# Optimization experiments

Measured on AMD Instinct MI355X. Metric: run time of the kernel, lower is better.

The kernel has to match this reference:

```python
import jax, jax.numpy as jnp
import numpy as np

B, N, EDGES = 16, 50000, 1600000
CLAMP_MIN, CLAMP_MAX = -10.0, 10.0
EPS = 1e-6


def setup_inputs() -> dict:
    key = jax.random.key(0)
    ks = jax.random.split(key, 8)
    return {
        "chem_influence": jax.random.normal(ks[0], (B, N), dtype=jnp.float32),
        "E": jax.random.normal(ks[1], (B, N), dtype=jnp.float32),
        "o_pre": jax.random.uniform(ks[2], (B, N), dtype=jnp.float32),
        "w": jax.random.normal(ks[3], (EDGES,), dtype=jnp.float32),
        "threshold": jax.random.uniform(ks[4], (N,), dtype=jnp.float32),
        "decay": jax.random.uniform(ks[5], (N,), dtype=jnp.float32),
        "src": jax.random.randint(ks[6], (EDGES,), 0, N, dtype=jnp.int32),
        "dst": jax.random.randint(ks[7], (EDGES,), 0, N, dtype=jnp.int32),
    }


def reference(chem_influence, E, o_pre, w, threshold, decay, src, dst):
    # Gap-junction currents: gather, sign-compare, weighted scatter-add.
    Oj = o_pre[:, src]                      # (B, EDGES) presynaptic outputs
    En = E[:, dst]                          # (B, EDGES) postsynaptic internal states
    sgn = jnp.where(Oj >= En, 1.0, -1.0)
    contrib = Oj * w * sgn                  # (B, EDGES)
    gj_sum = jnp.zeros_like(chem_influence).at[:, dst].add(contrib)  # (B, N)

    # Neuron dynamics (eqs 10, 11).
    S = jnp.clip(E + chem_influence + gj_sum, CLAMP_MIN, CLAMP_MAX)
    gt = S > threshold                      # broadcast (N,) over (B, N)
    mask = (~gt) & (jnp.abs(S - E) <= EPS)
    new_o = jax.nn.relu(S - threshold)
    new_e = jnp.where(gt, new_o, jnp.where(mask, E - decay, S))
    return (new_o, new_e)
```

## Files before the change

kernel.cpp:

```cpp
#include <hip/hip_runtime.h>

#define BATCH 16
#define NNODES 50000
#define NEDGES 1600000
#define BN (BATCH * NNODES)
#define NBLK 391
#define EPB 4096
#define BSZ 128
#define NBINS 391
#define CAPE 4992
#define RPT 10
#define CLAMP_LO -10.0f
#define CLAMP_HI 10.0f
#define EPS_V 1e-6f

__global__ __launch_bounds__(256) void prep_hist_kernel(
    const float* __restrict__ o_pre, const float* __restrict__ E,
    const int* __restrict__ dst,
    float* __restrict__ o_t, float* __restrict__ E_t,
    int* __restrict__ hist) {
    __shared__ int lh[NBINS];
    const int tid = threadIdx.x, bid = blockIdx.x;
    for (int i = tid; i < NBINS; i += 256) lh[i] = 0;

    if (tid < 128) {
        int t = bid * 128 + tid;
        if (t < NNODES) {
            float v[BATCH], u[BATCH];
#pragma unroll
            for (int b = 0; b < BATCH; ++b) {
                v[b] = o_pre[b * NNODES + t];
                u[b] = E[b * NNODES + t];
            }
            float4* op = (float4*)(o_t + (size_t)t * BATCH);
            float4* ep = (float4*)(E_t + (size_t)t * BATCH);
#pragma unroll
            for (int k = 0; k < 4; ++k) {
                op[k] = make_float4(v[4 * k], v[4 * k + 1], v[4 * k + 2], v[4 * k + 3]);
                ep[k] = make_float4(u[4 * k], u[4 * k + 1], u[4 * k + 2], u[4 * k + 3]);
            }
        }
    }
    __syncthreads();

    const int4* dst4 = (const int4*)dst;
    const int e4base = bid * (EPB / 4);
#pragma unroll
    for (int j = 0; j < 4; ++j) {
        int i4 = e4base + j * 256 + tid;
        if (i4 * 4 < NEDGES) {
            int4 d4 = dst4[i4];
            atomicAdd(&lh[d4.x >> 7], 1);
            atomicAdd(&lh[d4.y >> 7], 1);
            atomicAdd(&lh[d4.z >> 7], 1);
            atomicAdd(&lh[d4.w >> 7], 1);
        }
    }
    __syncthreads();
    for (int i = tid; i < NBINS; i += 256) hist[i * NBLK + bid] = lh[i];
}

__global__ __launch_bounds__(256) void scanA_kernel(int* __restrict__ hist,
                                                    int* __restrict__ totals) {
    __shared__ int sm[256];
    const int k = blockIdx.x, t = threadIdx.x;
    const int base = t * 2;
    int v0 = (base < NBLK) ? hist[k * NBLK + base] : 0;
    int v1 = (base + 1 < NBLK) ? hist[k * NBLK + base + 1] : 0;
    sm[t] = v0 + v1;
    __syncthreads();
    for (int off = 1; off < 256; off <<= 1) {
        int a = (t >= off) ? sm[t - off] : 0;
        __syncthreads();
        sm[t] += a;
        __syncthreads();
    }
    int run = (t > 0) ? sm[t - 1] : 0;
    if (base < NBLK) { hist[k * NBLK + base] = run; run += v0; }
    if (base + 1 < NBLK) hist[k * NBLK + base + 1] = run;
    if (t == 255) totals[k] = sm[255];
}

__global__ __launch_bounds__(256) void scatterA_kernel(
    const int* __restrict__ src, const int* __restrict__ dst,
    const float* __restrict__ w, const int* __restrict__ hist,
    uint2* __restrict__ binned) {
    __shared__ int cur[NBINS];
    const int tid = threadIdx.x, bid = blockIdx.x;
    for (int i = tid; i < NBINS; i += 256)
        cur[i] = i * CAPE + hist[i * NBLK + bid];
    __syncthreads();
    const int4*   dst4 = (const int4*)dst;
    const int4*   src4 = (const int4*)src;
    const float4* w4   = (const float4*)w;
    const int e4base = bid * (EPB / 4);
#pragma unroll
    for (int j = 0; j < 4; ++j) {
        int i4 = e4base + j * 256 + tid;
        if (i4 * 4 < NEDGES) {
            int4 d4 = dst4[i4];
            int4 s4 = src4[i4];
            float4 ww = w4[i4];
            int dd[4] = {d4.x, d4.y, d4.z, d4.w};
            int ss[4] = {s4.x, s4.y, s4.z, s4.w};
            float wv[4] = {ww.x, ww.y, ww.z, ww.w};
#pragma unroll
            for (int m = 0; m < 4; ++m) {
                int d = dd[m];
                int bin = d >> 7;
                int pos = atomicAdd(&cur[bin], 1);
                if (pos < (bin + 1) * CAPE)
                    binned[pos] = make_uint2(
                        (unsigned)ss[m] | ((unsigned)(d & 127) << 16),
                        __float_as_uint(wv[m]));
            }
        }
    }
}

__global__ __launch_bounds__(512) void bin_gather5(
    const float* __restrict__ o_t, const float* __restrict__ E_t,
    const float* __restrict__ chem, const float* __restrict__ threshold,
    const float* __restrict__ decay, const int* __restrict__ totals,
    const uint2* __restrict__ binned,
    float* __restrict__ out_o, float* __restrict__ out_e) {
    __shared__ int   cnt_l[BSZ];
    __shared__ int   offs[BSZ + 1];
    __shared__ int   sc[BSZ];
    __shared__ uint2 eb[CAPE];
    const int k = blockIdx.x, tid = threadIdx.x;
    const int node0 = k * BSZ;
    const int nn = (NNODES - node0 < BSZ) ? (NNODES - node0) : BSZ;
    const int s0 = k * CAPE;
    int cnt = totals[k];
    if (cnt > CAPE) cnt = CAPE;

    uint2 r[RPT];
    if (tid < BSZ) cnt_l[tid] = 0;
    __syncthreads();
#pragma unroll
    for (int j = 0; j < RPT; ++j) {
        int idx = tid + j * 512;
        if (idx < cnt) {
            uint2 p = binned[s0 + idx];
            r[j] = p;
            atomicAdd(&cnt_l[(p.x >> 16) & 127], 1);
        }
    }
    __syncthreads();

    if (tid < BSZ) sc[tid] = cnt_l[tid];
    __syncthreads();
    for (int o = 1; o < BSZ; o <<= 1) {
        int v = (tid >= o && tid < BSZ) ? sc[tid - o] : 0;
        __syncthreads();
        if (tid < BSZ) sc[tid] += v;
        __syncthreads();
    }
    if (tid < BSZ) {
        int ex = sc[tid] - cnt_l[tid];
        offs[tid] = ex;
        cnt_l[tid] = ex;
    }
    if (tid == 0) offs[BSZ] = cnt;
    __syncthreads();

#pragma unroll
    for (int j = 0; j < RPT; ++j) {
        int idx = tid + j * 512;
        if (idx < cnt) {
            uint2 p = r[j];
            int pos = atomicAdd(&cnt_l[(p.x >> 16) & 127], 1);
            if (pos < CAPE) eb[pos] = p;
        }
    }
    __syncthreads();

    for (int t = tid; t < nn * 4; t += 512) {
        int n = t >> 2;
        int q = (t & 3) * 4;
        int gn = node0 + n;
        int e0 = offs[n], e1 = offs[n + 1];
        float4 en = *(const float4*)(E_t + (size_t)gn * BATCH + q);
        float4 acc = make_float4(0.f, 0.f, 0.f, 0.f);
        for (int i = e0; i < e1; ++i) {
            uint2 p = eb[i];
            float wv = __uint_as_float(p.y);
            int s = (int)(p.x & 0xFFFFu);
            float4 oj = *(const float4*)(o_t + (size_t)s * BATCH + q);
            acc.x += (oj.x >= en.x) ? oj.x * wv : -oj.x * wv;
            acc.y += (oj.y >= en.y) ? oj.y * wv : -oj.y * wv;
            acc.z += (oj.z >= en.z) ? oj.z * wv : -oj.z * wv;
            acc.w += (oj.w >= en.w) ? oj.w * wv : -oj.w * wv;
        }
        float th = threshold[gn];
        float dc = decay[gn];
        float ev[4] = {en.x, en.y, en.z, en.w};
        float av[4] = {acc.x, acc.y, acc.z, acc.w};
#pragma unroll
        for (int j = 0; j < 4; ++j) {
            int b = q + j;
            float e = ev[j];
            float S = e + chem[b * NNODES + gn] + av[j];
            S = fminf(fmaxf(S, CLAMP_LO), CLAMP_HI);
            float no = fmaxf(S - th, 0.0f);
            float ne;
            if (S > th) ne = no;
            else if (fabsf(S - e) <= EPS_V) ne = e - dc;
            else ne = S;
            out_o[b * NNODES + gn] = no;
            out_e[b * NNODES + gn] = ne;
        }
    }
}

__global__ void edge_scatter_dev(const float* __restrict__ o_pre, const float* __restrict__ E,
                                 const float* __restrict__ w, const int* __restrict__ src,
                                 const int* __restrict__ dst, float* __restrict__ gj) {
    int e = blockIdx.x * blockDim.x + threadIdx.x;
    if (e >= NEDGES) return;
    int s = src[e];
    int d = dst[e];
    float wv = w[e];
#pragma unroll
    for (int b = 0; b < BATCH; ++b) {
        float oj = o_pre[b * NNODES + s];
        float en = E[b * NNODES + d];
        atomicAdd(&gj[b * NNODES + d], (oj >= en) ? oj * wv : -oj * wv);
    }
}

__global__ void finalize_dev(const float* __restrict__ chem, const float* __restrict__ E,
                             const float* __restrict__ threshold, const float* __restrict__ decay,
                             float* __restrict__ out_o, float* __restrict__ out_e_gj) {
    int i = blockIdx.x * blockDim.x + threadIdx.x;
    if (i >= BN) return;
    int n = i % NNODES;
    float e = E[i];
    float S = e + chem[i] + out_e_gj[i];
    S = fminf(fmaxf(S, CLAMP_LO), CLAMP_HI);
    float th = threshold[n];
    float no = fmaxf(S - th, 0.0f);
    float ne;
    if (S > th) ne = no;
    else if (fabsf(S - e) <= EPS_V) ne = e - decay[n];
    else ne = S;
    out_o[i] = no;
    out_e_gj[i] = ne;
}

extern "C" void kernel_launch(void* const* d_in, const int* in_sizes, int n_in,
                              void* d_out, int out_size, void* d_ws, size_t ws_size,
                              hipStream_t stream) {
    const float* chem      = (const float*)d_in[0];
    const float* E         = (const float*)d_in[1];
    const float* o_pre     = (const float*)d_in[2];
    const float* w         = (const float*)d_in[3];
    const float* threshold = (const float*)d_in[4];
    const float* decay     = (const float*)d_in[5];
    const int*   src       = (const int*)d_in[6];
    const int*   dst       = (const int*)d_in[7];

    float* out_o = (float*)d_out;
    float* out_e = (float*)d_out + BN;

    const size_t OT_OFF  = 0;
    const size_t ET_OFF  = 3200000;
    const size_t BIN_OFF = 6400000;
    const size_t H_OFF   = 22014976;
    const size_t TOT_OFF = 22626512;
    const size_t need    = TOT_OFF + (size_t)NBINS * sizeof(int);

    if (ws_size >= need) {
        char* ws = (char*)d_ws;
        float* o_t    = (float*)(ws + OT_OFF);
        float* E_t    = (float*)(ws + ET_OFF);
        uint2* binned = (uint2*)(ws + BIN_OFF);
        int*   hist   = (int*)(ws + H_OFF);
        int*   totals = (int*)(ws + TOT_OFF);

        prep_hist_kernel<<<NBLK, 256, 0, stream>>>(o_pre, E, dst, o_t, E_t, hist);
        scanA_kernel<<<NBINS, 256, 0, stream>>>(hist, totals);
        scatterA_kernel<<<NBLK, 256, 0, stream>>>(src, dst, w, hist, binned);
        bin_gather5<<<NBINS, 512, 0, stream>>>(o_t, E_t, chem, threshold, decay,
                                               totals, binned, out_o, out_e);
    } else {
        hipMemsetAsync(out_e, 0, (size_t)BN * sizeof(float), stream);
        edge_scatter_dev<<<(NEDGES + 255) / 256, 256, 0, stream>>>(o_pre, E, w, src, dst, out_e);
        finalize_dev<<<(BN + 255) / 256, 256, 0, stream>>>(chem, E, threshold, decay, out_o, out_e);
    }
}
```

Before: 131.5 us.

## Fuse histogram, scan and scatter via global atomic bin cursors; halve bin size

After: 125.3 us. -4.8%, faster.

```diff
diff --git a/kernel.cpp b/kernel.cpp
--- a/kernel.cpp
+++ b/kernel.cpp
@@ -4,24 +4,40 @@
 #define NNODES 50000
 #define NEDGES 1600000
 #define BN (BATCH * NNODES)
-#define NBLK 391
-#define EPB 4096
-#define BSZ 128
-#define NBINS 391
-#define CAPE 4992
-#define RPT 10
 #define CLAMP_LO -10.0f
 #define CLAMP_HI 10.0f
 #define EPS_V 1e-6f
 
-__global__ __launch_bounds__(256) void prep_hist_kernel(
+#define BSZ 64
+#define NBINS 782
+#define CAPE 2816
+#define RPT 11
+#define NBLK_P 391
+#define EPB 4096
+
+__global__ __launch_bounds__(256) void prep_fused(
     const float* __restrict__ o_pre, const float* __restrict__ E,
-    const int* __restrict__ dst,
+    const int* __restrict__ src, const int* __restrict__ dst,
+    const float* __restrict__ w,
     float* __restrict__ o_t, float* __restrict__ E_t,
-    int* __restrict__ hist) {
+    uint2* __restrict__ binned, int* __restrict__ gcur) {
     __shared__ int lh[NBINS];
     const int tid = threadIdx.x, bid = blockIdx.x;
     for (int i = tid; i < NBINS; i += 256) lh[i] = 0;
+
+    const int4*   dst4 = (const int4*)dst;
+    const int4*   src4 = (const int4*)src;
+    const float4* w4   = (const float4*)w;
+    const int e4base = bid * (EPB / 4);
+    int4 d[4], s[4];
+    float4 ww[4];
+    bool val[4];
+#pragma unroll
+    for (int j = 0; j < 4; ++j) {
+        int i4 = e4base + j * 256 + tid;
+        val[j] = (i4 * 4 < NEDGES);
+        if (val[j]) { d[j] = dst4[i4]; s[j] = src4[i4]; ww[j] = w4[i4]; }
+    }
 
     if (tid < 128) {
         int t = bid * 128 + tid;
@@ -36,103 +52,65 @@
             float4* ep = (float4*)(E_t + (size_t)t * BATCH);
 #pragma unroll
             for (int k = 0; k < 4; ++k) {
-                op[k] = make_float4(v[4 * k], v[4 * k + 1], v[4 * k + 2], v[4 * k + 3]);
-                ep[k] = make_float4(u[4 * k], u[4 * k + 1], u[4 * k + 2], u[4 * k + 3]);
+                op[k] = make_float4(v[4*k], v[4*k+1], v[4*k+2], v[4*k+3]);
+                ep[k] = make_float4(u[4*k], u[4*k+1], u[4*k+2], u[4*k+3]);
             }
         }
     }
     __syncthreads();
 
-    const int4* dst4 = (const int4*)dst;
-    const int e4base = bid * (EPB / 4);
 #pragma unroll
     for (int j = 0; j < 4; ++j) {
-        int i4 = e4base + j * 256 + tid;
-        if (i4 * 4 < NEDGES) {
-            int4 d4 = dst4[i4];
-            atomicAdd(&lh[d4.x >> 7], 1);
-            atomicAdd(&lh[d4.y >> 7], 1);
-            atomicAdd(&lh[d4.z >> 7], 1);
-            atomicAdd(&lh[d4.w >> 7], 1);
-        }
-    }
-    __syncthreads();
-    for (int i = tid; i < NBINS; i += 256) hist[i * NBLK + bid] = lh[i];
-}
-
-__global__ __launch_bounds__(256) void scanA_kernel(int* __restrict__ hist,
-                                                    int* __restrict__ totals) {
-    __shared__ int sm[256];
-    const int k = blockIdx.x, t = threadIdx.x;
-    const int base = t * 2;
-    int v0 = (base < NBLK) ? hist[k * NBLK + base] : 0;
-    int v1 = (base + 1 < NBLK) ? hist[k * NBLK + base + 1] : 0;
-    sm[t] = v0 + v1;
-    __syncthreads();
-    for (int off = 1; off < 256; off <<= 1) {
-        int a = (t >= off) ? sm[t - off] : 0;
-        __syncthreads();
-        sm[t] += a;
-        __syncthreads();
-    }
-    int run = (t > 0) ? sm[t - 1] : 0;
-    if (base < NBLK) { hist[k * NBLK + base] = run; run += v0; }
-    if (base + 1 < NBLK) hist[k * NBLK + base + 1] = run;
-    if (t == 255) totals[k] = sm[255];
-}
-
-__global__ __launch_bounds__(256) void scatterA_kernel(
-    const int* __restrict__ src, const int* __restrict__ dst,
-    const float* __restrict__ w, const int* __restrict__ hist,
-    uint2* __restrict__ binned) {
-    __shared__ int cur[NBINS];
-    const int tid = threadIdx.x, bid = blockIdx.x;
-    for (int i = tid; i < NBINS; i += 256)
-        cur[i] = i * CAPE + hist[i * NBLK + bid];
-    __syncthreads();
-    const int4*   dst4 = (const int4*)dst;
-    const int4*   src4 = (const int4*)src;
-    const float4* w4   = (const float4*)w;
-    const int e4base = bid * (EPB / 4);
+        if (val[j]) {
+            atomicAdd(&lh[d[j].x >> 6], 1);
+            atomicAdd(&lh[d[j].y >> 6], 1);
+            atomicAdd(&lh[d[j].z >> 6], 1);
+            atomicAdd(&lh[d[j].w >> 6], 1);
+        }
+    }
+    __syncthreads();
+
+    for (int i = tid; i < NBINS; i += 256) {
+        int c = lh[i];
+        int base = c ? atomicAdd(&gcur[i], c) : 0;
+        lh[i] = i * CAPE + base;
+    }
+    __syncthreads();
+
 #pragma unroll
     for (int j = 0; j < 4; ++j) {
-        int i4 = e4base + j * 256 + tid;
-        if (i4 * 4 < NEDGES) {
-            int4 d4 = dst4[i4];
-            int4 s4 = src4[i4];
-            float4 ww = w4[i4];
-            int dd[4] = {d4.x, d4.y, d4.z, d4.w};
-            int ss[4] = {s4.x, s4.y, s4.z, s4.w};
-            float wv[4] = {ww.x, ww.y, ww.z, ww.w};
+        if (val[j]) {
+            int   dd[4] = {d[j].x, d[j].y, d[j].z, d[j].w};
+            int   ss[4] = {s[j].x, s[j].y, s[j].z, s[j].w};
+            float wv[4] = {ww[j].x, ww[j].y, ww[j].z, ww[j].w};
 #pragma unroll
             for (int m = 0; m < 4; ++m) {
-                int d = dd[m];
-                int bin = d >> 7;
-                int pos = atomicAdd(&cur[bin], 1);
+                int dn  = dd[m];
+                int bin = dn >> 6;
+                int pos = atomicAdd(&lh[bin], 1);
                 if (pos < (bin + 1) * CAPE)
                     binned[pos] = make_uint2(
-                        (unsigned)ss[m] | ((unsigned)(d & 127) << 16),
+                        (unsigned)ss[m] | ((unsigned)(dn & 63) << 16),
                         __float_as_uint(wv[m]));
             }
         }
     }
 }
 
-__global__ __launch_bounds__(512) void bin_gather5(
+__global__ __launch_bounds__(256, 4) void bin_gather6(
     const float* __restrict__ o_t, const float* __restrict__ E_t,
     const float* __restrict__ chem, const float* __restrict__ threshold,
-    const float* __restrict__ decay, const int* __restrict__ totals,
+    const float* __restrict__ decay, const int* __restrict__ gcur,
     const uint2* __restrict__ binned,
     float* __restrict__ out_o, float* __restrict__ out_e) {
     __shared__ int   cnt_l[BSZ];
     __shared__ int   offs[BSZ + 1];
-    __shared__ int   sc[BSZ];
     __shared__ uint2 eb[CAPE];
     const int k = blockIdx.x, tid = threadIdx.x;
     const int node0 = k * BSZ;
     const int nn = (NNODES - node0 < BSZ) ? (NNODES - node0) : BSZ;
     const int s0 = k * CAPE;
-    int cnt = totals[k];
+    int cnt = gcur[k];
     if (cnt > CAPE) cnt = CAPE;
 
     uint2 r[RPT];
@@ -140,76 +118,94 @@
     __syncthreads();
 #pragma unroll
     for (int j = 0; j < RPT; ++j) {
-        int idx = tid + j * 512;
+        int idx = tid + j * 256;
         if (idx < cnt) {
             uint2 p = binned[s0 + idx];
             r[j] = p;
-            atomicAdd(&cnt_l[(p.x >> 16) & 127], 1);
-        }
-    }
-    __syncthreads();
-
-    if (tid < BSZ) sc[tid] = cnt_l[tid];
-    __syncthreads();
-    for (int o = 1; o < BSZ; o <<= 1) {
-        int v = (tid >= o && tid < BSZ) ? sc[tid - o] : 0;
-        __syncthreads();
-        if (tid < BSZ) sc[tid] += v;
-        __syncthreads();
-    }
+            atomicAdd(&cnt_l[(p.x >> 16) & 63], 1);
+        }
+    }
+    __syncthreads();
+
     if (tid < BSZ) {
-        int ex = sc[tid] - cnt_l[tid];
-        offs[tid] = ex;
-        cnt_l[tid] = ex;
-    }
-    if (tid == 0) offs[BSZ] = cnt;
+        int c = cnt_l[tid];
+        int v = c;
+#pragma unroll
+        for (int o = 1; o < BSZ; o <<= 1) {
+            int u = __shfl_up(v, o);
+            if (tid >= o) v += u;
+        }
+        offs[tid]  = v - c;
+        cnt_l[tid] = v - c;
+        if (tid == BSZ - 1) offs[BSZ] = cnt;
+    }
     __syncthreads();
 
 #pragma unroll
     for (int j = 0; j < RPT; ++j) {
-        int idx = tid + j * 512;
+        int idx = tid + j * 256;
         if (idx < cnt) {
             uint2 p = r[j];
-            int pos = atomicAdd(&cnt_l[(p.x >> 16) & 127], 1);
-            if (pos < CAPE) eb[pos] = p;
-        }
-    }
-    __syncthreads();
-
-    for (int t = tid; t < nn * 4; t += 512) {
-        int n = t >> 2;
-        int q = (t & 3) * 4;
-        int gn = node0 + n;
-        int e0 = offs[n], e1 = offs[n + 1];
-        float4 en = *(const float4*)(E_t + (size_t)gn * BATCH + q);
+            int pos = atomicAdd(&cnt_l[(p.x >> 16) & 63], 1);
+            eb[pos] = p;
+        }
+    }
+    __syncthreads();
+
+    if (tid < nn * 4) {
+        const int n  = tid >> 2;
+        const int q  = (tid & 3) * 4;
+        const int gn = node0 + n;
+        const int e0 = offs[n], e1 = offs[n + 1];
+        const float4 en = *(const float4*)(E_t + (size_t)gn * BATCH + q);
+        const float th = threshold[gn];
+        const float dc = decay[gn];
+        float ch[4];
+#pragma unroll
+        for (int j = 0; j < 4; ++j) ch[j] = chem[(q + j) * NNODES + gn];
+
         float4 acc = make_float4(0.f, 0.f, 0.f, 0.f);
-        for (int i = e0; i < e1; ++i) {
-            uint2 p = eb[i];
-            float wv = __uint_as_float(p.y);
-            int s = (int)(p.x & 0xFFFFu);
-            float4 oj = *(const float4*)(o_t + (size_t)s * BATCH + q);
-            acc.x += (oj.x >= en.x) ? oj.x * wv : -oj.x * wv;
-            acc.y += (oj.y >= en.y) ? oj.y * wv : -oj.y * wv;
-            acc.z += (oj.z >= en.z) ? oj.z * wv : -oj.z * wv;
-            acc.w += (oj.w >= en.w) ? oj.w * wv : -oj.w * wv;
-        }
-        float th = threshold[gn];
-        float dc = decay[gn];
+        int i = e0;
+        for (; i + 2 <= e1; i += 2) {
+            uint2 p0 = eb[i];
+            uint2 p1 = eb[i + 1];
+            float4 oj0 = *(const float4*)(o_t + (size_t)(p0.x & 0xFFFFu) * BATCH + q);
+            float4 oj1 = *(const float4*)(o_t + (size_t)(p1.x & 0xFFFFu) * BATCH + q);
+            float w0 = __uint_as_float(p0.y), nw0 = -w0;
+            float w1 = __uint_as_float(p1.y), nw1 = -w1;
+            acc.x = fmaf(oj0.x, (oj0.x >= en.x) ? w0 : nw0, acc.x);
+            acc.y = fmaf(oj0.y, (oj0.y >= en.y) ? w0 : nw0, acc.y);
+            acc.z = fmaf(oj0.z, (oj0.z >= en.z) ? w0 : nw0, acc.z);
+            acc.w = fmaf(oj0.w, (oj0.w >= en.w) ? w0 : nw0, acc.w);
+            acc.x = fmaf(oj1.x, (oj1.x >= en.x) ? w1 : nw1, acc.x);
+            acc.y = fmaf(oj1.y, (oj1.y >= en.y) ? w1 : nw1, acc.y);
+            acc.z = fmaf(oj1.z, (oj1.z >= en.z) ? w1 : nw1, acc.z);
+            acc.w = fmaf(oj1.w, (oj1.w >= en.w) ? w1 : nw1, acc.w);
+        }
+        if (i < e1) {
+            uint2 p0 = eb[i];
+            float4 oj0 = *(const float4*)(o_t + (size_t)(p0.x & 0xFFFFu) * BATCH + q);
+            float w0 = __uint_as_float(p0.y), nw0 = -w0;
+            acc.x = fmaf(oj0.x, (oj0.x >= en.x) ? w0 : nw0, acc.x);
+            acc.y = fmaf(oj0.y, (oj0.y >= en.y) ? w0 : nw0, acc.y);
+            acc.z = fmaf(oj0.z, (oj0.z >= en.z) ? w0 : nw0, acc.z);
+            acc.w = fmaf(oj0.w, (oj0.w >= en.w) ? w0 : nw0, acc.w);
+        }
+
         float ev[4] = {en.x, en.y, en.z, en.w};
         float av[4] = {acc.x, acc.y, acc.z, acc.w};
 #pragma unroll
         for (int j = 0; j < 4; ++j) {
-            int b = q + j;
             float e = ev[j];
-            float S = e + chem[b * NNODES + gn] + av[j];
+            float S = e + ch[j] + av[j];
             S = fminf(fmaxf(S, CLAMP_LO), CLAMP_HI);
             float no = fmaxf(S - th, 0.0f);
             float ne;
             if (S > th) ne = no;
             else if (fabsf(S - e) <= EPS_V) ne = e - dc;
             else ne = S;
-            out_o[b * NNODES + gn] = no;
-            out_e[b * NNODES + gn] = ne;
+            out_o[(q + j) * NNODES + gn] = no;
+            out_e[(q + j) * NNODES + gn] = ne;
         }
     }
 }
@@ -265,25 +261,22 @@
     float* out_e = (float*)d_out + BN;
 
     const size_t OT_OFF  = 0;
-    const size_t ET_OFF  = 3200000;
-    const size_t BIN_OFF = 6400000;
-    const size_t H_OFF   = 22014976;
-    const size_t TOT_OFF = 22626512;
-    const size_t need    = TOT_OFF + (size_t)NBINS * sizeof(int);
+    const size_t ET_OFF  = 3203072;
+    const size_t BIN_OFF = 6406144;
+    const size_t GC_OFF  = 24023040;
+    const size_t need    = GC_OFF + (size_t)NBINS * sizeof(int);
 
     if (ws_size >= need) {
         char* ws = (char*)d_ws;
         float* o_t    = (float*)(ws + OT_OFF);
         float* E_t    = (float*)(ws + ET_OFF);
         uint2* binned = (uint2*)(ws + BIN_OFF);
-        int*   hist   = (int*)(ws + H_OFF);
-        int*   totals = (int*)(ws + TOT_OFF);
-
-        prep_hist_kernel<<<NBLK, 256, 0, stream>>>(o_pre, E, dst, o_t, E_t, hist);
-        scanA_kernel<<<NBINS, 256, 0, stream>>>(hist, totals);
-        scatterA_kernel<<<NBLK, 256, 0, stream>>>(src, dst, w, hist, binned);
-        bin_gather5<<<NBINS, 512, 0, stream>>>(o_t, E_t, chem, threshold, decay,
-                                               totals, binned, out_o, out_e);
+        int*   gcur   = (int*)(ws + GC_OFF);
+
+        hipMemsetAsync(gcur, 0, (size_t)NBINS * sizeof(int), stream);
+        prep_fused<<<NBLK_P, 256, 0, stream>>>(o_pre, E, src, dst, w, o_t, E_t, binned, gcur);
+        bin_gather6<<<NBINS, 256, 0, stream>>>(o_t, E_t, chem, threshold, decay,
+                                               gcur, binned, out_o, out_e);
     } else {
         hipMemsetAsync(out_e, 0, (size_t)BN * sizeof(float), stream);
         edge_scatter_dev<<<(NEDGES + 255) / 256, 256, 0, stream>>>(o_pre, E, w, src, dst, out_e);
```
